# Performance work log

Hardware: AMD Instinct MI355X
Metric: run time of the kernel (lower is better)

The kernel has to match this reference:

```python
import jax, jax.numpy as jnp
import numpy as np

B, L, S, V, I, H = 4096, 16, 512, 512, 512, 512  # batch, attn_length, attn_size, attn_vec_size, input_size, lstm hidden


def setup_inputs() -> dict:
    key = jax.random.key(0)
    ks = jax.random.split(key, 16)
    rn = lambda k, sh, sc=1.0: jax.random.normal(k, sh, dtype=jnp.float32) * sc
    return {
        "inputs": rn(ks[0], (B, I)),
        "cell_c": rn(ks[1], (B, H)),
        "cell_h": rn(ks[2], (B, H)),
        "attns": rn(ks[3], (B, S)),
        "attn_states": rn(ks[4], (B, L, S)),
        "W1": rn(ks[5], (I + S, I), 0.02),
        "b1": jnp.zeros((I,), jnp.float32),
        "Wx": rn(ks[6], (I, 4 * H), 0.02),
        "Wh": rn(ks[7], (H, 4 * H), 0.02),
        "b_lstm": jnp.zeros((4 * H,), jnp.float32),
        "W3": rn(ks[8], (2 * H, V), 0.02),
        "b3": jnp.zeros((V,), jnp.float32),
        "k": rn(ks[9], (1, 1, S, V), 0.02),
        "v": rn(ks[10], (1, 1, S, V), 0.02),
        "W2": rn(ks[11], (H + S, S), 0.02),
        "b2": jnp.zeros((S,), jnp.float32),
    }


def reference(inputs, cell_c, cell_h, attns, attn_states, W1, b1, Wx, Wh, b_lstm, W3, b3, k, v, W2, b2):
    # linear1: project [inputs; attns] -> cell input
    x = jnp.concatenate([inputs, attns], axis=1) @ W1 + b1  # [B, I]
    # LSTM cell step (gate order i, f, g, o)
    gates = x @ Wx + cell_h @ Wh + b_lstm  # [B, 4H]
    i, f, g, o = jnp.split(gates, 4, axis=1)
    c_new = jax.nn.sigmoid(f) * cell_c + jax.nn.sigmoid(i) * jnp.tanh(g)
    h_new = jax.nn.sigmoid(o) * jnp.tanh(c_new)
    # attention over attn_states with query = concat(new_state)
    query = jnp.concatenate([c_new, h_new], axis=1)  # [B, 2H]
    # 1x1 conv over [B, L, 1, S] with kernel [1,1,S,V] == matmul over S
    hf = jnp.einsum('bls,sv->blv', attn_states, k[0, 0])  # [B, L, V]
    y = query @ W3 + b3  # [B, V]
    t = jnp.tanh(hf + y[:, None, :])  # [B, L, V]
    # reduce_sum(v * t, [2,3]) with v [1,1,S,V] broadcast against t [B,L,1,V]
    # == einsum over V with v summed over its S axis (t independent of S axis)
    vsum = v[0, 0].sum(axis=0)  # [V]
    s = jnp.einsum('blv,v->bl', t, vsum)  # [B, L]
    a = jax.nn.softmax(s, axis=1)
    d = jnp.einsum('bl,bls->bs', a, attn_states)  # new_attns [B, S]
    # output projection on [cell_output; new_attns]
    output = jnp.concatenate([h_new, d], axis=1) @ W2 + b2  # [B, S]
    # shift attention window: drop oldest, append output
    new_attn_states = jnp.concatenate([attn_states[:, 1:, :], output[:, None, :]], axis=1)
    new_attn_states = new_attn_states.reshape(inputs.shape[0], L * S)
    return output, c_new, h_new, d, new_attn_states
```

## Files before the change

kernel.cpp:

```cpp
#include <hip/hip_runtime.h>
#include <hip/hip_bf16.h>
#include <math.h>

#define BB 4096
#define LL 16
#define SS 512
#define VV 512
#define II 512
#define HH 512

typedef __attribute__((ext_vector_type(4))) float f32x4;
typedef __attribute__((ext_vector_type(8))) short short8;

#define GLOBAL_AS __attribute__((address_space(1)))
#define LDS_AS __attribute__((address_space(3)))

__device__ __forceinline__ unsigned short f2bf(float f) {
    union { float f; unsigned u; } c; c.f = f;
    unsigned u = c.u + 0x7FFFu + ((c.u >> 16) & 1u);
    return (unsigned short)(u >> 16);
}
__device__ __forceinline__ float bf2f(unsigned short u) {
    union { unsigned u; float f; } c; c.u = ((unsigned)u) << 16;
    return c.f;
}
__device__ __forceinline__ float fast_tanh(float x) {
    return 1.f - 2.f / (__expf(2.f * x) + 1.f);
}

template<int MODE, int NF>
__global__ __launch_bounds__(256) void gemm_mfma(
    const ushort* __restrict__ A, const ushort* __restrict__ Bt,
    const float* __restrict__ bias, void* __restrict__ C, float* __restrict__ C2,
    int ldc, int M, int N, int K) {
    constexpr int BN = NF * 32;
    __shared__ ushort Als[128 * 64];
    __shared__ ushort Bls[BN * 64];
    const int tid  = threadIdx.x;
    const int lane = tid & 63;
    const int w    = tid >> 6;
    const int wm   = w >> 1, wn = w & 1;
    const int brow = blockIdx.y * 128;
    const int bcol = blockIdx.x * BN;
    f32x4 acc[4][NF] = {};
    const int nkt = K >> 6;
    for (int kt = 0; kt < nkt; ++kt) {
        __syncthreads();
        #pragma unroll
        for (int i = 0; i < 4; ++i) {
            int c0 = i * 256 + w * 64;
            int c  = c0 + lane;
            int row = c >> 3, sl = c & 7;
            const ushort* gp = A + (size_t)(brow + row) * K + kt * 64 + ((sl ^ (row & 7)) * 8);
            __builtin_amdgcn_global_load_lds((const GLOBAL_AS void*)gp,
                                             (LDS_AS void*)(Als + c0 * 8), 16, 0, 0);
        }
        #pragma unroll
        for (int i = 0; i < NF; ++i) {
            int c0 = i * 256 + w * 64;
            int c  = c0 + lane;
            int row = c >> 3, sl = c & 7;
            const ushort* gp = Bt + (size_t)(bcol + row) * K + kt * 64 + ((sl ^ (row & 7)) * 8);
            __builtin_amdgcn_global_load_lds((const GLOBAL_AS void*)gp,
                                             (LDS_AS void*)(Bls + c0 * 8), 16, 0, 0);
        }
        __syncthreads();
        const char* AlsB = (const char*)Als;
        const char* BlsB = (const char*)Bls;
        #pragma unroll
        for (int kh = 0; kh < 2; ++kh) {
            int ks = kh * 4 + (lane >> 4);
            short8 a[4], b[NF];
            #pragma unroll
            for (int m = 0; m < 4; ++m) {
                int row = wm * 64 + m * 16 + (lane & 15);
                a[m] = *(const short8*)(AlsB + (row * 8 + (ks ^ (row & 7))) * 16);
            }
            #pragma unroll
            for (int n = 0; n < NF; ++n) {
                int row = wn * (NF * 16) + n * 16 + (lane & 15);
                b[n] = *(const short8*)(BlsB + (row * 8 + (ks ^ (row & 7))) * 16);
            }
            #pragma unroll
            for (int m = 0; m < 4; ++m)
                #pragma unroll
                for (int n = 0; n < NF; ++n)
                    acc[m][n] = __builtin_amdgcn_mfma_f32_16x16x32_bf16(a[m], b[n], acc[m][n], 0, 0, 0);
        }
    }
    #pragma unroll
    for (int m = 0; m < 4; ++m)
        #pragma unroll
        for (int n = 0; n < NF; ++n)
            #pragma unroll
            for (int r = 0; r < 4; ++r) {
                int gm = brow + wm * 64 + m * 16 + (lane >> 4) * 4 + r;
                int gc = bcol + wn * (NF * 16) + n * 16 + (lane & 15);
                float v = acc[m][n][r] + bias[gc];
                if (MODE == 1) ((ushort*)C)[(size_t)gm * ldc + gc] = f2bf(v);
                else           ((float*)C)[(size_t)gm * ldc + gc] = v;
                if (MODE == 2) C2[((size_t)gm * 16 + 15) * 512 + gc] = v;
            }
}

__global__ __launch_bounds__(256) void gemm_gates(
    const ushort* __restrict__ A, const ushort* __restrict__ Bt,
    const float* __restrict__ bias, const float* __restrict__ cc,
    float* __restrict__ o_c, float* __restrict__ o_h,
    ushort* __restrict__ A4, ushort* __restrict__ A7) {
    __shared__ ushort Als[128 * 64];
    __shared__ ushort Bls[64 * 64];
    const int tid = threadIdx.x, lane = tid & 63, w = tid >> 6;
    const int l15 = lane & 15, l4 = lane >> 4;
    const int brow = blockIdx.y * 128;
    const int xb = blockIdx.x;
    f32x4 acc[2][4] = {};
    for (int kt = 0; kt < 16; ++kt) {
        __syncthreads();
        #pragma unroll
        for (int i = 0; i < 4; ++i) {
            int c0 = i * 256 + w * 64, c = c0 + lane;
            int row = c >> 3, sl = c & 7;
            const ushort* gp = A + (size_t)(brow + row) * 1024 + kt * 64 + ((sl ^ (row & 7)) * 8);
            __builtin_amdgcn_global_load_lds((const GLOBAL_AS void*)gp,
                                             (LDS_AS void*)(Als + c0 * 8), 16, 0, 0);
        }
        #pragma unroll
        for (int i = 0; i < 2; ++i) {
            int c0 = i * 256 + w * 64, c = c0 + lane;
            int row = c >> 3, sl = c & 7;
            const ushort* gp = Bt + (size_t)(xb * 64 + row) * 1024 + kt * 64 + ((sl ^ (row & 7)) * 8);
            __builtin_amdgcn_global_load_lds((const GLOBAL_AS void*)gp,
                                             (LDS_AS void*)(Bls + c0 * 8), 16, 0, 0);
        }
        __syncthreads();
        const char* AlsB = (const char*)Als;
        const char* BlsB = (const char*)Bls;
        #pragma unroll
        for (int kh = 0; kh < 2; ++kh) {
            int ks = kh * 4 + l4;
            short8 a[2], b[4];
            #pragma unroll
            for (int m = 0; m < 2; ++m) {
                int row = w * 32 + m * 16 + l15;
                a[m] = *(const short8*)(AlsB + (row * 8 + (ks ^ (row & 7))) * 16);
            }
            #pragma unroll
            for (int n = 0; n < 4; ++n) {
                int row = n * 16 + l15;
                b[n] = *(const short8*)(BlsB + (row * 8 + (ks ^ (row & 7))) * 16);
            }
            #pragma unroll
            for (int m = 0; m < 2; ++m)
                #pragma unroll
                for (int n = 0; n < 4; ++n)
                    acc[m][n] = __builtin_amdgcn_mfma_f32_16x16x32_bf16(a[m], b[n], acc[m][n], 0, 0, 0);
        }
    }
    const int h = xb * 16 + l15;
    #pragma unroll
    for (int m = 0; m < 2; ++m)
        #pragma unroll
        for (int r = 0; r < 4; ++r) {
            int gm = brow + w * 32 + m * 16 + l4 * 4 + r;
            float gi = acc[m][0][r] + bias[h];
            float gf = acc[m][1][r] + bias[512 + h];
            float gg = acc[m][2][r] + bias[1024 + h];
            float go = acc[m][3][r] + bias[1536 + h];
            float si = 1.f / (1.f + __expf(-gi));
            float sf = 1.f / (1.f + __expf(-gf));
            float so = 1.f / (1.f + __expf(-go));
            float cv = sf * cc[(size_t)gm * 512 + h] + si * tanhf(gg);
            float hn = so * tanhf(cv);
            o_c[(size_t)gm * 512 + h] = cv;
            o_h[(size_t)gm * 512 + h] = hn;
            A4[(size_t)gm * 1024 + h] = f2bf(cv);
            A4[(size_t)gm * 1024 + 512 + h] = f2bf(hn);
            A7[(size_t)gm * 1024 + h] = f2bf(hn);
        }
}

__global__ __launch_bounds__(512, 4) void score_all(
    const float* __restrict__ ASf, const ushort* __restrict__ Bt,
    const float* __restrict__ Y, const float* __restrict__ vsum,
    float* __restrict__ o_ns, float* __restrict__ o_d, ushort* __restrict__ A7) {
    __shared__ ushort Als[64 * 64];
    __shared__ ushort Bls[512 * 64];
    __shared__ float sred[8][64];
    __shared__ float s_lds[64];
    const int tid  = threadIdx.x;
    const int lane = tid & 63;
    const int w    = tid >> 6;
    const int l15  = lane & 15, l4 = lane >> 4;
    const int brow = blockIdx.x * 64;
    const int bg0  = brow >> 4;
    f32x4 acc[4][4] = {};
    for (int kt = 0; kt < 8; ++kt) {
        __syncthreads();
        #pragma unroll
        for (int i = 0; i < 8; ++i) {
            int c0 = i * 512 + w * 64;
            int c  = c0 + lane;
            int row = c >> 3, sl = c & 7;
            const ushort* gp = Bt + (size_t)row * 512 + kt * 64 + ((sl ^ (row & 7)) * 8);
            __builtin_amdgcn_global_load_lds((const GLOBAL_AS void*)gp,
                                             (LDS_AS void*)(Bls + c0 * 8), 16, 0, 0);
        }
        {
            int chunk = tid;
            int row = chunk >> 3, slot = chunk & 7;
            int gslot = slot ^ (row & 7);
            const float* gp = ASf + (size_t)(brow + row) * 512 + kt * 64 + gslot * 8;
            float4 f0 = *(const float4*)gp;
            float4 f1 = *(const float4*)(gp + 4);
            short8 pk;
            pk[0] = (short)f2bf(f0.x); pk[1] = (short)f2bf(f0.y);
            pk[2] = (short)f2bf(f0.z); pk[3] = (short)f2bf(f0.w);
            pk[4] = (short)f2bf(f1.x); pk[5] = (short)f2bf(f1.y);
            pk[6] = (short)f2bf(f1.z); pk[7] = (short)f2bf(f1.w);
            *(short8*)((char*)Als + chunk * 16) = pk;
        }
        __syncthreads();
        const char* AlsB = (const char*)Als;
        const char* BlsB = (const char*)Bls;
        #pragma unroll
        for (int kh = 0; kh < 2; ++kh) {
            int ks = kh * 4 + l4;
            short8 a[4], b[4];
            #pragma unroll
            for (int m = 0; m < 4; ++m) {
                int row = m * 16 + l15;
                a[m] = *(const short8*)(AlsB + (row * 8 + (ks ^ (row & 7))) * 16);
            }
            #pragma unroll
            for (int n = 0; n < 4; ++n) {
                int rowb = w * 64 + n * 16 + l15;
                b[n] = *(const short8*)(BlsB + (rowb * 8 + (ks ^ (rowb & 7))) * 16);
            }
            #pragma unroll
            for (int m = 0; m < 4; ++m)
                #pragma unroll
                for (int n = 0; n < 4; ++n)
                    acc[m][n] = __builtin_amdgcn_mfma_f32_16x16x32_bf16(a[m], b[n], acc[m][n], 0, 0, 0);
        }
    }
    float part[4][4] = {};
    #pragma unroll
    for (int m = 0; m < 4; ++m) {
        int yb = bg0 + m;
        #pragma unroll
        for (int n = 0; n < 4; ++n) {
            int gc = w * 64 + n * 16 + l15;
            float yv = Y[(size_t)yb * 512 + gc];
            float vs = vsum[gc];
            #pragma unroll
            for (int r = 0; r < 4; ++r)
                part[m][r] += fast_tanh(acc[m][n][r] + yv) * vs;
        }
    }
    #pragma unroll
    for (int m = 0; m < 4; ++m)
        #pragma unroll
        for (int r = 0; r < 4; ++r) {
            float v = part[m][r];
            v += __shfl_xor(v, 1); v += __shfl_xor(v, 2);
            v += __shfl_xor(v, 4); v += __shfl_xor(v, 8);
            if (l15 == 0) sred[w][m * 16 + l4 * 4 + r] = v;
        }
    __syncthreads();
    if (tid < 64) {
        float v = 0.f;
        #pragma unroll
        for (int q = 0; q < 8; ++q) v += sred[q][tid];
        s_lds[tid] = v;
    }
    __syncthreads();

    {
        const int bat = w >> 1;
        const int bg  = bg0 + bat;
        const int c   = (w & 1) * 256 + lane * 4;
        float mx = -1e30f;
        #pragma unroll
        for (int l = 0; l < LL; ++l) mx = fmaxf(mx, s_lds[bat * 16 + l]);
        float wgt[LL]; float sum = 0.f;
        #pragma unroll
        for (int l = 0; l < LL; ++l) { wgt[l] = __expf(s_lds[bat * 16 + l] - mx); sum += wgt[l]; }
        const float inv = 1.f / sum;
        float d0 = 0.f, d1 = 0.f, d2 = 0.f, d3 = 0.f;
        #pragma unroll
        for (int l = 0; l < LL; ++l) {
            float4 v = *(const float4*)(ASf + ((size_t)bg * 16 + l) * 512 + c);
            if (l >= 1)
                *(float4*)(o_ns + ((size_t)bg * 16 + l - 1) * 512 + c) = v;
            d0 += wgt[l] * v.x; d1 += wgt[l] * v.y;
            d2 += wgt[l] * v.z; d3 += wgt[l] * v.w;
        }
        d0 *= inv; d1 *= inv; d2 *= inv; d3 *= inv;
        float4 dv; dv.x = d0; dv.y = d1; dv.z = d2; dv.w = d3;
        *(float4*)(o_d + (size_t)bg * 512 + c) = dv;
        ushort4 uv; uv.x = f2bf(d0); uv.y = f2bf(d1); uv.z = f2bf(d2); uv.w = f2bf(d3);
        *(ushort4*)(A7 + (size_t)bg * 1024 + 512 + c) = uv;
    }
}

struct TrJob { const float* srcA; const float* srcB; int K0; ushort* dst; int N; int K; int perm; };
struct TrJobs { TrJob j[5]; };

__global__ void tr_cvt_all(TrJobs jobs) {
    TrJob jb = jobs.j[blockIdx.z];
    int bn = blockIdx.x, bk = blockIdx.y;
    if (bn * 32 >= jb.N || bk * 32 >= jb.K) return;
    __shared__ float tile[32][33];
    int tx = threadIdx.x, ty = threadIdx.y;
    #pragma unroll
    for (int j = 0; j < 4; ++j) {
        int k = bk * 32 + ty + j * 8;
        const float* s = (k < jb.K0) ? (jb.srcA + (size_t)k * jb.N)
                                     : (jb.srcB + (size_t)(k - jb.K0) * jb.N);
        tile[ty + j * 8][tx] = s[bn * 32 + tx];
    }
    __syncthreads();
    #pragma unroll
    for (int j = 0; j < 4; ++j) {
        int n = bn * 32 + ty + j * 8;
        int nd = n;
        if (jb.perm) {
            int g = n >> 9, u = n & 511;
            nd = (u >> 4) * 64 + g * 16 + (u & 15);
        }
        jb.dst[(size_t)nd * jb.K + bk * 32 + tx] = f2bf(tile[tx][ty + j * 8]);
    }
}

struct CvJobs { const float* src[3]; ushort* dst[3]; };
__global__ void cvt_all(CvJobs jobs) {
    const float* src = jobs.src[blockIdx.y];
    ushort* dst = jobs.dst[blockIdx.y];
    int idx = blockIdx.x * 256 + threadIdx.x;
    int i4 = idx & 127, row = idx >> 7;
    float4 v = *(const float4*)(src + (size_t)row * 512 + i4 * 4);
    ushort4 o; o.x = f2bf(v.x); o.y = f2bf(v.y); o.z = f2bf(v.z); o.w = f2bf(v.w);
    *(ushort4*)(dst + (size_t)row * 1024 + i4 * 4) = o;
}

__global__ void vsum_k(const float* __restrict__ Vm, float* __restrict__ out) {
    __shared__ float red[8][32];
    int tc = threadIdx.x & 31, ts = threadIdx.x >> 5;
    int v = blockIdx.x * 32 + tc;
    float acc = 0.f;
    for (int s = ts; s < SS; s += 8) acc += Vm[(size_t)s * VV + v];
    red[ts][tc] = acc;
    __syncthreads();
    if (ts == 0) {
        float t = 0.f;
        #pragma unroll
        for (int j = 0; j < 8; ++j) t += red[j][tc];
        out[v] = t;
    }
}

extern "C" void kernel_launch(void* const* d_in, const int* in_sizes, int n_in,
                              void* d_out, int out_size, void* d_ws, size_t ws_size,
                              hipStream_t stream) {
    const float* inputs      = (const float*)d_in[0];
    const float* cell_c      = (const float*)d_in[1];
    const float* cell_h      = (const float*)d_in[2];
    const float* attns       = (const float*)d_in[3];
    const float* attn_states = (const float*)d_in[4];
    const float* W1          = (const float*)d_in[5];
    const float* b1          = (const float*)d_in[6];
    const float* Wx          = (const float*)d_in[7];
    const float* Wh          = (const float*)d_in[8];
    const float* b_lstm      = (const float*)d_in[9];
    const float* W3          = (const float*)d_in[10];
    const float* b3          = (const float*)d_in[11];
    const float* kmat        = (const float*)d_in[12];
    const float* vmat        = (const float*)d_in[13];
    const float* W2          = (const float*)d_in[14];
    const float* b2          = (const float*)d_in[15];

    float* o_out = (float*)d_out;
    float* o_c   = o_out + (size_t)BB * HH;
    float* o_h   = o_c   + (size_t)BB * HH;
    float* o_d   = o_h   + (size_t)BB * HH;
    float* o_ns  = o_d   + (size_t)BB * SS;

    float* ws_y     = (float*)d_ws;
    float* ws_vsum  = ws_y + (size_t)BB * VV;
    ushort* A1    = (ushort*)(ws_vsum + VV);
    ushort* A2    = A1 + (size_t)BB * 1024;
    ushort* A4    = A2 + (size_t)BB * 1024;
    ushort* A7    = A4 + (size_t)BB * 1024;
    ushort* W1t   = A7 + (size_t)BB * 1024;
    ushort* WBt   = W1t + (size_t)512 * 1024;
    ushort* W3t   = WBt + (size_t)2048 * 1024;
    ushort* W2t   = W3t + (size_t)512 * 1024;
    ushort* kTt   = W2t + (size_t)512 * 1024;

    TrJobs tj;
    tj.j[0] = {W1, W1, 1024, W1t, 512, 1024, 0};
    tj.j[1] = {Wx, Wh, 512, WBt, 2048, 1024, 1};
    tj.j[2] = {W3, W3, 1024, W3t, 512, 1024, 0};
    tj.j[3] = {W2, W2, 1024, W2t, 512, 1024, 0};
    tj.j[4] = {kmat, kmat, 512, kTt, 512, 512, 0};
    tr_cvt_all<<<dim3(64, 32, 5), dim3(32, 8), 0, stream>>>(tj);
    CvJobs cj;
    cj.src[0] = inputs; cj.dst[0] = A1;
    cj.src[1] = attns;  cj.dst[1] = A1 + 512;
    cj.src[2] = cell_h; cj.dst[2] = A2 + 512;
    cvt_all<<<dim3(BB * 128 / 256, 3), 256, 0, stream>>>(cj);
    vsum_k<<<16, 256, 0, stream>>>(vmat, ws_vsum);

    gemm_mfma<1, 1><<<dim3(512 / 32, BB / 128), 256, 0, stream>>>(
        A1, W1t, b1, A2, nullptr, 1024, BB, 512, 1024);
    gemm_gates<<<dim3(32, BB / 128), 256, 0, stream>>>(
        A2, WBt, b_lstm, cell_c, o_c, o_h, A4, A7);
    gemm_mfma<0, 1><<<dim3(512 / 32, BB / 128), 256, 0, stream>>>(
        A4, W3t, b3, ws_y, nullptr, 512, BB, 512, 1024);
    score_all<<<BB * LL / 64, 512, 0, stream>>>(
        attn_states, kTt, ws_y, ws_vsum, o_ns, o_d, A7);
    gemm_mfma<2, 1><<<dim3(512 / 32, BB / 128), 256, 0, stream>>>(
        A7, W2t, b2, o_out, o_ns, 512, BB, 512, 1024);
}
```

Measured before the change: 226.8 us.

## Use 8-wave 512-thread GEMM blocks with wider N tiles and swizzle score blocks

The generic GEMM and the LSTM gates GEMM now run with 512 threads (8 waves in a 2x4 layout), doubling or quadrupling the N tile per block so each A tile loaded into LDS is reused across more columns. The gates kernel now covers 256 weight rows (64 hidden units across 4 gate groups) per block instead of 64. The score kernel remaps block indices with a stride-8 swizzle to change the order in which blocks visit memory. Together these halve or quarter the grid sizes, which may cut occupancy and wave-level parallelism in exchange for less redundant global and LDS traffic.

```diff
diff --git a/kernel.cpp b/kernel.cpp
--- a/kernel.cpp
+++ b/kernel.cpp
@@ -28,27 +28,28 @@
     return 1.f - 2.f / (__expf(2.f * x) + 1.f);
 }
 
-template<int MODE, int NF>
-__global__ __launch_bounds__(256) void gemm_mfma(
+template<int MODE, int NFW>
+__global__ __launch_bounds__(512) void gemm8(
     const ushort* __restrict__ A, const ushort* __restrict__ Bt,
     const float* __restrict__ bias, void* __restrict__ C, float* __restrict__ C2,
-    int ldc, int M, int N, int K) {
-    constexpr int BN = NF * 32;
+    int ldc, int K) {
+    constexpr int BN = NFW * 64;
     __shared__ ushort Als[128 * 64];
     __shared__ ushort Bls[BN * 64];
     const int tid  = threadIdx.x;
     const int lane = tid & 63;
     const int w    = tid >> 6;
-    const int wm   = w >> 1, wn = w & 1;
+    const int wm   = w >> 2, wn = w & 3;
+    const int l15  = lane & 15, l4 = lane >> 4;
     const int brow = blockIdx.y * 128;
     const int bcol = blockIdx.x * BN;
-    f32x4 acc[4][NF] = {};
+    f32x4 acc[4][NFW] = {};
     const int nkt = K >> 6;
     for (int kt = 0; kt < nkt; ++kt) {
         __syncthreads();
         #pragma unroll
-        for (int i = 0; i < 4; ++i) {
-            int c0 = i * 256 + w * 64;
+        for (int i = 0; i < 2; ++i) {
+            int c0 = i * 512 + w * 64;
             int c  = c0 + lane;
             int row = c >> 3, sl = c & 7;
             const ushort* gp = A + (size_t)(brow + row) * K + kt * 64 + ((sl ^ (row & 7)) * 8);
@@ -56,8 +57,8 @@
                                              (LDS_AS void*)(Als + c0 * 8), 16, 0, 0);
         }
         #pragma unroll
-        for (int i = 0; i < NF; ++i) {
-            int c0 = i * 256 + w * 64;
+        for (int i = 0; i < NFW; ++i) {
+            int c0 = i * 512 + w * 64;
             int c  = c0 + lane;
             int row = c >> 3, sl = c & 7;
             const ushort* gp = Bt + (size_t)(bcol + row) * K + kt * 64 + ((sl ^ (row & 7)) * 8);
@@ -69,33 +70,33 @@
         const char* BlsB = (const char*)Bls;
         #pragma unroll
         for (int kh = 0; kh < 2; ++kh) {
-            int ks = kh * 4 + (lane >> 4);
-            short8 a[4], b[NF];
+            int ks = kh * 4 + l4;
+            short8 a[4], b[NFW];
             #pragma unroll
             for (int m = 0; m < 4; ++m) {
-                int row = wm * 64 + m * 16 + (lane & 15);
+                int row = wm * 64 + m * 16 + l15;
                 a[m] = *(const short8*)(AlsB + (row * 8 + (ks ^ (row & 7))) * 16);
             }
             #pragma unroll
-            for (int n = 0; n < NF; ++n) {
-                int row = wn * (NF * 16) + n * 16 + (lane & 15);
+            for (int n = 0; n < NFW; ++n) {
+                int row = wn * (NFW * 16) + n * 16 + l15;
                 b[n] = *(const short8*)(BlsB + (row * 8 + (ks ^ (row & 7))) * 16);
             }
             #pragma unroll
             for (int m = 0; m < 4; ++m)
                 #pragma unroll
-                for (int n = 0; n < NF; ++n)
+                for (int n = 0; n < NFW; ++n)
                     acc[m][n] = __builtin_amdgcn_mfma_f32_16x16x32_bf16(a[m], b[n], acc[m][n], 0, 0, 0);
         }
     }
     #pragma unroll
     for (int m = 0; m < 4; ++m)
         #pragma unroll
-        for (int n = 0; n < NF; ++n)
+        for (int n = 0; n < NFW; ++n)
             #pragma unroll
             for (int r = 0; r < 4; ++r) {
-                int gm = brow + wm * 64 + m * 16 + (lane >> 4) * 4 + r;
-                int gc = bcol + wn * (NF * 16) + n * 16 + (lane & 15);
+                int gm = brow + wm * 64 + m * 16 + l4 * 4 + r;
+                int gc = bcol + wn * (NFW * 16) + n * 16 + l15;
                 float v = acc[m][n][r] + bias[gc];
                 if (MODE == 1) ((ushort*)C)[(size_t)gm * ldc + gc] = f2bf(v);
                 else           ((float*)C)[(size_t)gm * ldc + gc] = v;
@@ -103,33 +104,38 @@
             }
 }
 
-__global__ __launch_bounds__(256) void gemm_gates(
+__global__ __launch_bounds__(512) void gemm_gates8(
     const ushort* __restrict__ A, const ushort* __restrict__ Bt,
     const float* __restrict__ bias, const float* __restrict__ cc,
     float* __restrict__ o_c, float* __restrict__ o_h,
     ushort* __restrict__ A4, ushort* __restrict__ A7) {
     __shared__ ushort Als[128 * 64];
-    __shared__ ushort Bls[64 * 64];
-    const int tid = threadIdx.x, lane = tid & 63, w = tid >> 6;
-    const int l15 = lane & 15, l4 = lane >> 4;
+    __shared__ ushort Bls[256 * 64];
+    const int tid  = threadIdx.x;
+    const int lane = tid & 63;
+    const int w    = tid >> 6;
+    const int wm   = w >> 2, wn = w & 3;
+    const int l15  = lane & 15, l4 = lane >> 4;
     const int brow = blockIdx.y * 128;
-    const int xb = blockIdx.x;
-    f32x4 acc[2][4] = {};
+    const int xb   = blockIdx.x;
+    f32x4 acc[4][4] = {};
     for (int kt = 0; kt < 16; ++kt) {
         __syncthreads();
         #pragma unroll
-        for (int i = 0; i < 4; ++i) {
-            int c0 = i * 256 + w * 64, c = c0 + lane;
+        for (int i = 0; i < 2; ++i) {
+            int c0 = i * 512 + w * 64;
+            int c  = c0 + lane;
             int row = c >> 3, sl = c & 7;
             const ushort* gp = A + (size_t)(brow + row) * 1024 + kt * 64 + ((sl ^ (row & 7)) * 8);
             __builtin_amdgcn_global_load_lds((const GLOBAL_AS void*)gp,
                                              (LDS_AS void*)(Als + c0 * 8), 16, 0, 0);
         }
         #pragma unroll
-        for (int i = 0; i < 2; ++i) {
-            int c0 = i * 256 + w * 64, c = c0 + lane;
+        for (int i = 0; i < 4; ++i) {
+            int c0 = i * 512 + w * 64;
+            int c  = c0 + lane;
             int row = c >> 3, sl = c & 7;
-            const ushort* gp = Bt + (size_t)(xb * 64 + row) * 1024 + kt * 64 + ((sl ^ (row & 7)) * 8);
+            const ushort* gp = Bt + (size_t)(xb * 256 + row) * 1024 + kt * 64 + ((sl ^ (row & 7)) * 8);
             __builtin_amdgcn_global_load_lds((const GLOBAL_AS void*)gp,
                                              (LDS_AS void*)(Bls + c0 * 8), 16, 0, 0);
         }
@@ -139,30 +145,30 @@
         #pragma unroll
         for (int kh = 0; kh < 2; ++kh) {
             int ks = kh * 4 + l4;
-            short8 a[2], b[4];
-            #pragma unroll
-            for (int m = 0; m < 2; ++m) {
-                int row = w * 32 + m * 16 + l15;
+            short8 a[4], b[4];
+            #pragma unroll
+            for (int m = 0; m < 4; ++m) {
+                int row = wm * 64 + m * 16 + l15;
                 a[m] = *(const short8*)(AlsB + (row * 8 + (ks ^ (row & 7))) * 16);
             }
             #pragma unroll
             for (int n = 0; n < 4; ++n) {
-                int row = n * 16 + l15;
+                int row = wn * 64 + n * 16 + l15;
                 b[n] = *(const short8*)(BlsB + (row * 8 + (ks ^ (row & 7))) * 16);
             }
             #pragma unroll
-            for (int m = 0; m < 2; ++m)
+            for (int m = 0; m < 4; ++m)
                 #pragma unroll
                 for (int n = 0; n < 4; ++n)
                     acc[m][n] = __builtin_amdgcn_mfma_f32_16x16x32_bf16(a[m], b[n], acc[m][n], 0, 0, 0);
         }
     }
-    const int h = xb * 16 + l15;
-    #pragma unroll
-    for (int m = 0; m < 2; ++m)
+    const int h = (xb * 4 + wn) * 16 + l15;
+    #pragma unroll
+    for (int m = 0; m < 4; ++m)
         #pragma unroll
         for (int r = 0; r < 4; ++r) {
-            int gm = brow + w * 32 + m * 16 + l4 * 4 + r;
+            int gm = brow + wm * 64 + m * 16 + l4 * 4 + r;
             float gi = acc[m][0][r] + bias[h];
             float gf = acc[m][1][r] + bias[512 + h];
             float gg = acc[m][2][r] + bias[1024 + h];
@@ -192,7 +198,9 @@
     const int lane = tid & 63;
     const int w    = tid >> 6;
     const int l15  = lane & 15, l4 = lane >> 4;
-    const int brow = blockIdx.x * 64;
+    const int bid  = blockIdx.x;
+    const int swz  = (bid & 7) * (BB * LL / 64 / 8) + (bid >> 3);
+    const int brow = swz * 64;
     const int bg0  = brow >> 4;
     f32x4 acc[4][4] = {};
     for (int kt = 0; kt < 8; ++kt) {
@@ -412,14 +420,14 @@
     cvt_all<<<dim3(BB * 128 / 256, 3), 256, 0, stream>>>(cj);
     vsum_k<<<16, 256, 0, stream>>>(vmat, ws_vsum);
 
-    gemm_mfma<1, 1><<<dim3(512 / 32, BB / 128), 256, 0, stream>>>(
-        A1, W1t, b1, A2, nullptr, 1024, BB, 512, 1024);
-    gemm_gates<<<dim3(32, BB / 128), 256, 0, stream>>>(
+    gemm8<1, 1><<<dim3(512 / 64, BB / 128), 512, 0, stream>>>(
+        A1, W1t, b1, A2, nullptr, 1024, 1024);
+    gemm_gates8<<<dim3(2048 / 256, BB / 128), 512, 0, stream>>>(
         A2, WBt, b_lstm, cell_c, o_c, o_h, A4, A7);
-    gemm_mfma<0, 1><<<dim3(512 / 32, BB / 128), 256, 0, stream>>>(
-        A4, W3t, b3, ws_y, nullptr, 512, BB, 512, 1024);
+    gemm8<0, 1><<<dim3(512 / 64, BB / 128), 512, 0, stream>>>(
+        A4, W3t, b3, ws_y, nullptr, 512, 1024);
     score_all<<<BB * LL / 64, 512, 0, stream>>>(
         attn_states, kTt, ws_y, ws_vsum, o_ns, o_d, A7);
-    gemm_mfma<2, 1><<<dim3(512 / 32, BB / 128), 256, 0, stream>>>(
-        A7, W2t, b2, o_out, o_ns, 512, BB, 512, 1024);
-}
+    gemm8<2, 1><<<dim3(512 / 64, BB / 128), 512, 0, stream>>>(
+        A7, W2t, b2, o_out, o_ns, 512, 1024);
+}
```

Result: slower. 237.1 us (+4.5%).
